# Performance work log

Measured on AMD Instinct MI355X. Metric: run time of the kernel, lower is better.

The kernel has to match this reference:

```python
import jax, jax.numpy as jnp
import numpy as np

B, T, INP, HID, ACT = 64, 1000, 64, 512, 2

def setup_inputs() -> dict:
    key = jax.random.key(0)
    k1, k2, k3, k4, k5 = jax.random.split(key, 5)
    s_hh = (6.0 / (HID + HID)) ** 0.5  # xavier_uniform bounds
    s_ih = (6.0 / (INP + HID)) ** 0.5
    s_fc = (6.0 / (HID + ACT)) ** 0.5
    return {
        "inp": jax.random.normal(k1, (B, T, INP), dtype=jnp.float32),
        "hn": jax.random.normal(k2, (1, B, HID), dtype=jnp.float32),
        "W_hh": jax.random.uniform(k3, (HID, HID), jnp.float32, -s_hh, s_hh),
        "W_ih": jax.random.uniform(k4, (INP, HID), jnp.float32, -s_ih, s_ih),
        "W_fc": jax.random.uniform(k5, (HID, ACT), jnp.float32, -s_fc, s_fc),
        "b_fc": jnp.zeros((ACT,), dtype=jnp.float32),
    }

def reference(inp, hn, W_hh, W_ih, W_fc, b_fc):
    # Precompute input projections for all timesteps in one big GEMM: [B,T,H]
    inp_proj = jnp.einsum("bti,ih->bth", inp, W_ih)
    h0 = hn[0]  # [B, H]

    def step(h, x_t):
        h_next = jax.nn.sigmoid(h @ W_hh + x_t)
        return h_next, h_next

    # scan over time: xs must be time-major
    _, hs = jax.lax.scan(step, h0, jnp.swapaxes(inp_proj, 0, 1))
    rnn_out = jnp.swapaxes(hs, 0, 1)  # [B, T, H]
    hn_last = rnn_out[:, -1, :][None]  # [1, B, H]
    out = jax.nn.sigmoid(rnn_out @ W_fc + b_fc)  # [B, T, ACT]
    return (out, hn_last, rnn_out)
```

## Files before the change

### kernel.cpp

```cpp
#include <hip/hip_runtime.h>
#include <hip/hip_bf16.h>
#include <stdint.h>
#include <math.h>

#define B   64
#define T   1000
#define INP 64
#define HID 512
#define ACT 2

#define NSLICE 4
#define MROWS  2
#define NGROUP (B / MROWS)
#define NBLOCKS (NGROUP * NSLICE)
#define COLS   (HID / NSLICE)
#define HLPAD  544

#define FAST_GUARD 1024

typedef __attribute__((ext_vector_type(8))) short short8;
typedef __attribute__((ext_vector_type(4))) float floatx4;

__device__ __forceinline__ uint64_t l2_load64(const uint64_t* p) {
  uint64_t v;
  asm volatile("global_load_dwordx2 %0, %1, off sc0\n\t"
               "s_waitcnt vmcnt(0)"
               : "=v"(v) : "v"(p) : "memory");
  return v;
}
__device__ __forceinline__ void l2_store64(uint64_t* p, uint64_t v) {
  asm volatile("global_store_dwordx2 %0, %1, off"
               :: "v"(p), "v"(v) : "memory");
}

__global__ __launch_bounds__(256) void init_kernel(
    const float* __restrict__ hn, uint64_t* __restrict__ h_fast,
    uint64_t* __restrict__ h_safe) {
  const int i   = blockIdx.x * 256 + threadIdx.x;
  const int g   = i >> 9;
  const int col = i & (HID - 1);
  __hip_bfloat16 b0 = __float2bfloat16(hn[(2 * g) * HID + col]);
  __hip_bfloat16 b1 = __float2bfloat16(hn[(2 * g + 1) * HID + col]);
  const uint32_t w0 = ((uint32_t)*reinterpret_cast<unsigned short*>(&b0)) << 16;
  const uint32_t w1 = ((uint32_t)*reinterpret_cast<unsigned short*>(&b1)) << 16;
  const uint64_t v  = (uint64_t)w0 | ((uint64_t)w1 << 32);
  const size_t p1 = (size_t)NGROUP * HID + i;
  h_fast[p1] = v;
  h_safe[p1] = v;
  h_fast[i] = 0x0000FFFE0000FFFEull;
  h_safe[i] = 0x0000FFFE0000FFFEull;
}

__global__ __launch_bounds__(256) void xproj_kernel(
    const float* __restrict__ inp, const float* __restrict__ W_ih,
    float* __restrict__ rnn) {
  __shared__ float xin[16 * INP];
  const int tid = threadIdx.x;
  const long r0 = (long)blockIdx.x * 16;

  const float4* inp4 = (const float4*)(inp + r0 * INP);
  ((float4*)xin)[tid] = inp4[tid];
  __syncthreads();

  const int j = tid, j2 = tid + 256;
  float acc0[16], acc1[16];
#pragma unroll
  for (int r = 0; r < 16; ++r) { acc0[r] = 0.f; acc1[r] = 0.f; }

  for (int i = 0; i < INP; ++i) {
    const float w0 = W_ih[i * HID + j];
    const float w1 = W_ih[i * HID + j2];
#pragma unroll
    for (int r = 0; r < 16; ++r) {
      const float x = xin[r * INP + i];
      acc0[r] = fmaf(x, w0, acc0[r]);
      acc1[r] = fmaf(x, w1, acc1[r]);
    }
  }
#pragma unroll
  for (int r = 0; r < 16; ++r) {
    rnn[(r0 + r) * HID + j]  = acc0[r];
    rnn[(r0 + r) * HID + j2] = acc1[r];
  }
}

__global__ __launch_bounds__(512) void rnn_mfma(
    const float* __restrict__ W_hh, float* __restrict__ rnn,
    float* __restrict__ hn_out, uint64_t* __restrict__ h_fast,
    uint64_t* __restrict__ h_safe) {
  __shared__ __align__(16) unsigned short hl[2][MROWS][HLPAD];

  const int tid  = threadIdx.x;
  const int lane = tid & 63;
  const int w    = tid >> 6;
  const int g    = blockIdx.x & (NGROUP - 1);
  const int s    = blockIdx.x >> 5;
  const int r0   = g * MROWS;
  const int n_base = s * COLS + w * 16;

  const int lm = lane & 15;
  const int lq = lane >> 4;
  const int cc = n_base + lm;

  short8 bfrag[16];
#pragma unroll
  for (int kt = 0; kt < 16; ++kt) {
    short8 f;
#pragma unroll
    for (int i = 0; i < 8; ++i) {
      const int k = kt * 32 + lq * 8 + i;
      __hip_bfloat16 hb = __float2bfloat16(W_hh[k * HID + cc]);
      f[i] = *reinterpret_cast<short*>(&hb);
    }
    bfrag[kt] = f;
  }

  const int  arow   = lm & 1;
  const bool remote = ((tid >> 7) != s);
  const bool prod   = (lq == 0);

  long ro0 = ((long)r0 * T + 0) * HID + cc;
  long ro1 = ((long)(r0 + 1) * T + 0) * HID + cc;
  float xp0 = 0.f, xp1 = 0.f;
  if (prod) { xp0 = rnn[ro0]; xp1 = rnn[ro1]; }

  int fastmode = 1;

  for (int t = 0; t < T; ++t) {
    const int p = (t + 1) & 1;

    if (t == 0 || remote) {
      const size_t idx = ((size_t)p * NGROUP + g) * HID + tid;
      const uint64_t want = (uint64_t)(t & 0xFFFF) * 0x0000000100000001ull;
      uint64_t v = 0;
      if (fastmode) {
        int ok = 0;
        for (int it = 0; it < FAST_GUARD; ++it) {
          v = l2_load64(h_fast + idx);
          if (((v ^ want) & 0x0000FFFF0000FFFFull) == 0) { ok = 1; break; }
        }
        if (!ok) fastmode = 0;
      }
      if (!fastmode) {
        int guard = 0;
        for (;;) {
          v = __hip_atomic_load(h_safe + idx, __ATOMIC_RELAXED,
                                __HIP_MEMORY_SCOPE_AGENT);
          if (((v ^ want) & 0x0000FFFF0000FFFFull) == 0) break;
          if (++guard > (1 << 20)) break;
        }
      }
      hl[p][0][tid] = (unsigned short)((uint32_t)v >> 16);
      hl[p][1][tid] = (unsigned short)((uint32_t)(v >> 32) >> 16);
    }
    __syncthreads();

    float nxp0 = 0.f, nxp1 = 0.f;
    long nro0 = ro0, nro1 = ro1;
    if (prod && t + 1 < T) {
      nro0 = ro0 + HID; nro1 = ro1 + HID;
      nxp0 = rnn[nro0]; nxp1 = rnn[nro1];
    }

    floatx4 c0 = {0.f, 0.f, 0.f, 0.f}, c1 = c0, c2 = c0, c3 = c0;
    const unsigned short* ap = &hl[p][arow][lq * 8];
#pragma unroll
    for (int kt = 0; kt < 16; kt += 4) {
      short8 a0 = *(const short8*)(ap + (kt + 0) * 32);
      short8 a1 = *(const short8*)(ap + (kt + 1) * 32);
      short8 a2 = *(const short8*)(ap + (kt + 2) * 32);
      short8 a3 = *(const short8*)(ap + (kt + 3) * 32);
      c0 = __builtin_amdgcn_mfma_f32_16x16x32_bf16(a0, bfrag[kt + 0], c0, 0, 0, 0);
      c1 = __builtin_amdgcn_mfma_f32_16x16x32_bf16(a1, bfrag[kt + 1], c1, 0, 0, 0);
      c2 = __builtin_amdgcn_mfma_f32_16x16x32_bf16(a2, bfrag[kt + 2], c2, 0, 0, 0);
      c3 = __builtin_amdgcn_mfma_f32_16x16x32_bf16(a3, bfrag[kt + 3], c3, 0, 0, 0);
    }

    if (prod) {
      const float z0 = c0[0] + c1[0] + c2[0] + c3[0] + xp0;
      const float z1 = c0[1] + c1[1] + c2[1] + c3[1] + xp1;
      const float h0 = 1.f / (1.f + __expf(-z0));
      const float h1 = 1.f / (1.f + __expf(-z1));
      __hip_bfloat16 b0 = __float2bfloat16(h0);
      __hip_bfloat16 b1 = __float2bfloat16(h1);
      const unsigned short u0 = *reinterpret_cast<unsigned short*>(&b0);
      const unsigned short u1 = *reinterpret_cast<unsigned short*>(&b1);

      const uint32_t tag = (uint32_t)(t + 1) & 0xFFFFu;
      const uint64_t word =
          (uint64_t)(((uint32_t)u0 << 16) | tag) |
          ((uint64_t)(((uint32_t)u1 << 16) | tag) << 32);
      const size_t didx = ((size_t)(t & 1) * NGROUP + g) * HID + cc;
      l2_store64(h_fast + didx, word);
      __hip_atomic_store(h_safe + didx, word, __ATOMIC_RELAXED,
                         __HIP_MEMORY_SCOPE_AGENT);

      hl[t & 1][0][cc] = u0;
      hl[t & 1][1][cc] = u1;

      rnn[ro0] = h0;
      rnn[ro1] = h1;
      if (t == T - 1) {
        hn_out[r0 * HID + cc]       = h0;
        hn_out[(r0 + 1) * HID + cc] = h1;
      }
      xp0 = nxp0; xp1 = nxp1; ro0 = nro0; ro1 = nro1;
    }
  }
}

__global__ __launch_bounds__(256) void fc_kernel(
    const float* __restrict__ rnn, const float* __restrict__ W_fc,
    const float* __restrict__ b_fc, float* __restrict__ out) {
  const int lane = threadIdx.x & 63;
  const int wid  = threadIdx.x >> 6;
  const long row = (long)blockIdx.x * 4 + wid;

  const float4* __restrict__ hrow = (const float4*)(rnn + row * HID);
  const float4* __restrict__ Wfc4 = (const float4*)W_fc;

  float a0 = 0.f, a1 = 0.f;
#pragma unroll
  for (int u = 0; u < 2; ++u) {
    const float4 hv = hrow[lane * 2 + u];
    const int j0 = lane * 8 + u * 4;
    const float4 wA = Wfc4[(j0 >> 1)];
    const float4 wB = Wfc4[(j0 >> 1) + 1];
    a0 += hv.x * wA.x + hv.y * wA.z + hv.z * wB.x + hv.w * wB.z;
    a1 += hv.x * wA.y + hv.y * wA.w + hv.z * wB.y + hv.w * wB.w;
  }
#pragma unroll
  for (int off = 32; off > 0; off >>= 1) {
    a0 += __shfl_down(a0, off, 64);
    a1 += __shfl_down(a1, off, 64);
  }
  if (lane == 0) {
    out[row * 2 + 0] = 1.f / (1.f + __expf(-(a0 + b_fc[0])));
    out[row * 2 + 1] = 1.f / (1.f + __expf(-(a1 + b_fc[1])));
  }
}

extern "C" void kernel_launch(void* const* d_in, const int* in_sizes, int n_in,
                              void* d_out, int out_size, void* d_ws,
                              size_t ws_size, hipStream_t stream) {
  const float* inp  = (const float*)d_in[0];
  const float* hn   = (const float*)d_in[1];
  const float* W_hh = (const float*)d_in[2];
  const float* W_ih = (const float*)d_in[3];
  const float* W_fc = (const float*)d_in[4];
  const float* b_fc = (const float*)d_in[5];

  float* out    = (float*)d_out;
  float* hn_out = out + (long)B * T * ACT;
  float* rnn    = hn_out + (long)B * HID;

  uint64_t* h_fast = (uint64_t*)d_ws;
  const size_t HCNT = (size_t)2 * NGROUP * HID;
  uint64_t* h_safe =
      (ws_size >= 2 * HCNT * sizeof(uint64_t)) ? (h_fast + HCNT) : h_fast;

  hipLaunchKernelGGL(init_kernel, dim3((NGROUP * HID) / 256), dim3(256), 0,
                     stream, hn, h_fast, h_safe);
  hipLaunchKernelGGL(xproj_kernel, dim3((B * T) / 16), dim3(256), 0, stream,
                     inp, W_ih, rnn);
  hipLaunchKernelGGL(rnn_mfma, dim3(NBLOCKS), dim3(512), 0, stream,
                     W_hh, rnn, hn_out, h_fast, h_safe);
  hipLaunchKernelGGL(fc_kernel, dim3((B * T) / 4), dim3(256), 0, stream,
                     rnn, W_fc, b_fc, out);
}
```

Before: 1.794 ms.

## Assign RNN work groups to blocks by XCD so each group shares one L2

The recurrent kernel now launches 256 blocks. Each block reads its hardware XCC id and claims a slot through per-XCD atomic counters, so the four column slices of one batch group all land on the same XCD and exchange hidden state through a shared L2. If every work item is claimed, blocks use the fast mode. Otherwise they fall back to the old blockIdx mapping, and surplus blocks exit. The fast-spin guard is also lowered. The cost is an all-block arrival barrier at startup, and the kernel relies on all 256 blocks being co-resident.

```diff
diff --git a/kernel.cpp b/kernel.cpp
--- a/kernel.cpp
+++ b/kernel.cpp
@@ -13,10 +13,12 @@
 #define MROWS  2
 #define NGROUP (B / MROWS)
 #define NBLOCKS (NGROUP * NSLICE)
+#define NLAUNCH 256
+#define WORK_PER_XCD 16
 #define COLS   (HID / NSLICE)
 #define HLPAD  544
 
-#define FAST_GUARD 1024
+#define FAST_GUARD 256
 
 typedef __attribute__((ext_vector_type(8))) short short8;
 typedef __attribute__((ext_vector_type(4))) float floatx4;
@@ -32,10 +34,18 @@
   asm volatile("global_store_dwordx2 %0, %1, off"
                :: "v"(p), "v"(v) : "memory");
 }
+__device__ __forceinline__ int get_xcc_id() {
+  int x;
+  asm volatile("s_getreg_b32 %0, hwreg(HW_REG_XCC_ID)" : "=s"(x));
+  return x & 7;
+}
+
+#define CTRL_WORDS 16
 
 __global__ __launch_bounds__(256) void init_kernel(
     const float* __restrict__ hn, uint64_t* __restrict__ h_fast,
-    uint64_t* __restrict__ h_safe) {
+    uint64_t* __restrict__ h_safe, uint32_t* __restrict__ ctrl) {
+  if (blockIdx.x == 0 && threadIdx.x < CTRL_WORDS) ctrl[threadIdx.x] = 0;
   const int i   = blockIdx.x * 256 + threadIdx.x;
   const int g   = i >> 9;
   const int col = i & (HID - 1);
@@ -87,14 +97,56 @@
 __global__ __launch_bounds__(512) void rnn_mfma(
     const float* __restrict__ W_hh, float* __restrict__ rnn,
     float* __restrict__ hn_out, uint64_t* __restrict__ h_fast,
-    uint64_t* __restrict__ h_safe) {
+    uint64_t* __restrict__ h_safe, uint32_t* __restrict__ ctrl) {
   __shared__ __align__(16) unsigned short hl[2][MROWS][HLPAD];
+  __shared__ int sh_g, sh_s, sh_work, sh_mode;
 
   const int tid  = threadIdx.x;
+
+  if (tid == 0) {
+    uint32_t* cnt      = ctrl;
+    uint32_t* claimed  = ctrl + 8;
+    uint32_t* arrivals = ctrl + 9;
+    uint32_t* flag     = ctrl + 10;
+    const int xcc = get_xcc_id();
+    const int slot = (int)__hip_atomic_fetch_add(
+        &cnt[xcc], 1u, __ATOMIC_RELAXED, __HIP_MEMORY_SCOPE_AGENT);
+    int work = 0, g = 0, s = 0;
+    if (slot < WORK_PER_XCD) {
+      g = xcc * 4 + (slot >> 2);
+      s = slot & 3;
+      work = 1;
+      __hip_atomic_fetch_add(claimed, 1u, __ATOMIC_RELEASE,
+                             __HIP_MEMORY_SCOPE_AGENT);
+    }
+    const int arr = (int)__hip_atomic_fetch_add(
+        arrivals, 1u, __ATOMIC_ACQ_REL, __HIP_MEMORY_SCOPE_AGENT);
+    if (arr == NLAUNCH - 1) {
+      const uint32_t c = __hip_atomic_load(claimed, __ATOMIC_ACQUIRE,
+                                           __HIP_MEMORY_SCOPE_AGENT);
+      __hip_atomic_store(flag, (c == NBLOCKS) ? 2u : 1u, __ATOMIC_RELEASE,
+                         __HIP_MEMORY_SCOPE_AGENT);
+    }
+    uint32_t f = 0; int guard = 0;
+    do {
+      f = __hip_atomic_load(flag, __ATOMIC_ACQUIRE, __HIP_MEMORY_SCOPE_AGENT);
+    } while (f == 0 && ++guard < (1 << 20));
+    if (f != 2) {
+      work = (blockIdx.x < NBLOCKS);
+      g = blockIdx.x & (NGROUP - 1);
+      s = blockIdx.x >> 5;
+    }
+    sh_g = g; sh_s = s; sh_work = work; sh_mode = (f == 2);
+  }
+  __syncthreads();
+  if (!sh_work) return;
+
+  const int g = __builtin_amdgcn_readfirstlane(sh_g);
+  const int s = __builtin_amdgcn_readfirstlane(sh_s);
+  int fastmode = __builtin_amdgcn_readfirstlane(sh_mode);
+
   const int lane = tid & 63;
   const int w    = tid >> 6;
-  const int g    = blockIdx.x & (NGROUP - 1);
-  const int s    = blockIdx.x >> 5;
   const int r0   = g * MROWS;
   const int n_base = s * COLS + w * 16;
 
@@ -123,8 +175,6 @@
   long ro1 = ((long)(r0 + 1) * T + 0) * HID + cc;
   float xp0 = 0.f, xp1 = 0.f;
   if (prod) { xp0 = rnn[ro0]; xp1 = rnn[ro1]; }
-
-  int fastmode = 1;
 
   for (int t = 0; t < T; ++t) {
     const int p = (t + 1) & 1;
@@ -254,17 +304,19 @@
   float* hn_out = out + (long)B * T * ACT;
   float* rnn    = hn_out + (long)B * HID;
 
-  uint64_t* h_fast = (uint64_t*)d_ws;
+  uint32_t* ctrl   = (uint32_t*)d_ws;
+  uint64_t* h_fast = (uint64_t*)((char*)d_ws + 256);
   const size_t HCNT = (size_t)2 * NGROUP * HID;
   uint64_t* h_safe =
-      (ws_size >= 2 * HCNT * sizeof(uint64_t)) ? (h_fast + HCNT) : h_fast;
+      (ws_size >= 256 + 2 * HCNT * sizeof(uint64_t)) ? (h_fast + HCNT)
+                                                     : h_fast;
 
   hipLaunchKernelGGL(init_kernel, dim3((NGROUP * HID) / 256), dim3(256), 0,
-                     stream, hn, h_fast, h_safe);
+                     stream, hn, h_fast, h_safe, ctrl);
   hipLaunchKernelGGL(xproj_kernel, dim3((B * T) / 16), dim3(256), 0, stream,
                      inp, W_ih, rnn);
-  hipLaunchKernelGGL(rnn_mfma, dim3(NBLOCKS), dim3(512), 0, stream,
-                     W_hh, rnn, hn_out, h_fast, h_safe);
+  hipLaunchKernelGGL(rnn_mfma, dim3(NLAUNCH), dim3(512), 0, stream,
+                     W_hh, rnn, hn_out, h_fast, h_safe, ctrl);
   hipLaunchKernelGGL(fc_kernel, dim3((B * T) / 4), dim3(256), 0, stream,
                      rnn, W_fc, b_fc, out);
 }
```

Measured after the change: 1.497 ms. 16.6% less time.
